# Kernel tuning notes

Measured on AMD Instinct MI355X. Metric: run time of the kernel, lower is better.

## Reference

```python
import jax, jax.numpy as jnp
import numpy as np

B, I, H = 16384, 512, 512


def setup_inputs() -> dict:
    key = jax.random.key(0)
    ks = jax.random.split(key, 10)
    inputs = jax.random.normal(ks[0], (B, I), dtype=jnp.float32)
    state = jax.random.normal(ks[1], (B, 2 * H), dtype=jnp.float32)
    # xavier_uniform for w_ih: U(-a, a), a = sqrt(6 / (fan_in + fan_out))
    a = float(np.sqrt(6.0 / (2 * H + I)))
    w_ih = jax.random.uniform(ks[2], (2 * H, I), jnp.float32, -a, a)
    b_h = jnp.zeros((H,), jnp.float32)
    pi = float(np.pi)
    d1 = jax.random.uniform(ks[3], (H,), jnp.float32, -pi, pi)
    d2 = jax.random.uniform(ks[4], (H,), jnp.float32, -pi, pi)
    d3 = jax.random.uniform(ks[5], (H,), jnp.float32, -pi, pi)
    re1 = jax.random.uniform(ks[6], (H,), jnp.float32, -1.0, 1.0)
    im1 = jax.random.uniform(ks[7], (H,), jnp.float32, -1.0, 1.0)
    re2 = jax.random.uniform(ks[8], (H,), jnp.float32, -1.0, 1.0)
    im2 = jax.random.uniform(ks[9], (H,), jnp.float32, -1.0, 1.0)
    perm = jnp.asarray(np.random.default_rng(0).permutation(H), dtype=jnp.int32)
    return {"inputs": inputs, "state": state, "w_ih": w_ih, "b_h": b_h,
            "d1": d1, "d2": d2, "d3": d3,
            "re1": re1, "im1": im1, "re2": re2, "im2": im2, "perm": perm}


def _diag_mul(w, z):
    # multiply by exp(i*w) built as complex(cos w, sin w), as in the original
    return jax.lax.complex(jnp.cos(w), jnp.sin(w)) * z


def _reflect(re, im, z):
    # z - (2/||v||^2) * (z @ conj(v)) outer v   (faithful to original matmuls)
    v = jax.lax.complex(re, im)                 # [H]
    vz = z @ jnp.conj(v)                        # [B]
    factor = 2.0 / jnp.sum(re * re + im * im)   # real scalar
    return z - factor * vz[:, None] * v[None, :]


def _modrelu(z, b):
    norm = jnp.abs(z)
    scale = jax.nn.relu(norm + b) / (norm + 1e-6)
    return z * scale


def reference(inputs, state, w_ih, b_h, d1, d2, d3, re1, im1, re2, im2, perm):
    inputs_mul = inputs @ w_ih.T                                  # [B, 2H]
    z_in = jax.lax.complex(inputs_mul[:, :H], inputs_mul[:, H:])  # [B, H] c64
    state_c = jax.lax.complex(state[:, :H], state[:, H:])
    # Unitary chain (computed in original forward, but its result `preact` is
    # never used for the returned state -- faithfully reproduced).
    s = _diag_mul(d1, state_c)
    s = jnp.fft.fft(s, axis=-1)
    s = _reflect(re1, im1, s)
    s = s[:, perm]                 # column permutation (z.T[P].T)
    s = _diag_mul(d2, s)
    s = jnp.fft.ifft(s, axis=-1)
    s = _reflect(re2, im2, s)
    s = _diag_mul(d3, s)
    preact = z_in + s              # dead in original; kept for fidelity
    new_state_c = _modrelu(z_in, b_h)
    return jnp.concatenate([jnp.real(new_state_c), jnp.imag(new_state_c)], axis=1)
```

## Files before the change

### kernel.cpp

```cpp
#include <hip/hip_runtime.h>
#include <hip/hip_bf16.h>


typedef __attribute__((ext_vector_type(8))) short bf16x8;
typedef __attribute__((ext_vector_type(4))) float f32x4;

#define BM 256
#define BK 64
#define KDIM 512
#define NDIM 1024
#define NKT (KDIM / BK)

__device__ __forceinline__ unsigned short f2bf(float f) {
    unsigned u = __builtin_bit_cast(unsigned, f);
    u += 0x7fffu + ((u >> 16) & 1u);
    return (unsigned short)(u >> 16);
}

__global__ __launch_bounds__(256) void cvt_both(
    const float* __restrict__ A, const float* __restrict__ W,
    unsigned short* __restrict__ Abf, unsigned short* __restrict__ Wbf,
    int nA4, int nTot4) {
    int i = blockIdx.x * blockDim.x + threadIdx.x;
    int stride = gridDim.x * blockDim.x;
    for (; i < nTot4; i += stride) {
        float4 v;
        if (i < nA4) v = reinterpret_cast<const float4*>(A)[i];
        else         v = reinterpret_cast<const float4*>(W)[i - nA4];
        ushort4 o;
        o.x = f2bf(v.x); o.y = f2bf(v.y); o.z = f2bf(v.z); o.w = f2bf(v.w);
        if (i < nA4) reinterpret_cast<ushort4*>(Abf)[i] = o;
        else         reinterpret_cast<ushort4*>(Wbf)[i - nA4] = o;
    }
}

__device__ __forceinline__ void gload_lds16(const void* g, void* l) {
    __builtin_amdgcn_global_load_lds(
        (const __attribute__((address_space(1))) unsigned int*)g,
        (__attribute__((address_space(3))) unsigned int*)l, 16, 0, 0);
}

__global__ __launch_bounds__(512, 2) void gemm_modrelu(
    const unsigned short* __restrict__ A,
    const unsigned short* __restrict__ W,
    const float* __restrict__ bh,
    float* __restrict__ out)
{
    __shared__ unsigned short At[2][BM * BK];
    __shared__ unsigned short Bt[2][BM * BK];

    const int tid = threadIdx.x;
    const int w   = tid >> 6;
    const int l   = tid & 63;
    const int l15 = l & 15;
    const int l4  = l >> 4;
    const int wm  = w >> 2;
    const int wn  = w & 3;

    const int bx = blockIdx.x;
    const int lg = (bx & 7) * 32 + (bx >> 3);
    const int mb = lg >> 2;
    const int cb = lg & 3;

    const int srow = l >> 3;
    const int sseg = (l & 7) ^ srow;

    const unsigned short* ga[4];
    const unsigned short* gb[4];
    int ldso[4];
#pragma unroll
    for (int is = 0; is < 4; ++is) {
        int row  = w * 32 + is * 8 + srow;
        ga[is]   = A + (size_t)(mb * BM + row) * KDIM + sseg * 8;
        int wrow = (row >> 7) * 512 + cb * 128 + (row & 127);
        gb[is]   = W + (size_t)wrow * KDIM + sseg * 8;
        ldso[is] = (w * 32 + is * 8) * BK;
    }

    f32x4 acc[8][4];
#pragma unroll
    for (int i = 0; i < 8; ++i)
#pragma unroll
        for (int j = 0; j < 4; ++j) acc[i][j] = f32x4{0.f, 0.f, 0.f, 0.f};

    auto stage = [&](int kt, int buf) {
#pragma unroll
        for (int is = 0; is < 4; ++is)
            gload_lds16(ga[is] + kt * BK, &At[buf][ldso[is]]);
#pragma unroll
        for (int is = 0; is < 4; ++is)
            gload_lds16(gb[is] + kt * BK, &Bt[buf][ldso[is]]);
    };

    stage(0, 0);
    stage(1, 1);
    asm volatile("s_waitcnt vmcnt(8)" ::: "memory");
    __builtin_amdgcn_s_barrier();

#pragma unroll
    for (int kt = 0; kt < NKT; ++kt) {
        const int buf = kt & 1;

#pragma unroll
        for (int ks = 0; ks < 2; ++ks) {
            bf16x8 af[8], bf[4];
            const int slot = (ks * 4 + l4) ^ (l15 & 7);
#pragma unroll
            for (int i = 0; i < 8; ++i) {
                int row = wm * 128 + i * 16 + l15;
                af[i] = *(const bf16x8*)(&At[buf][row * BK + slot * 8]);
            }
#pragma unroll
            for (int jn = 0; jn < 4; ++jn) {
                int row = (jn < 2) ? (wn * 32 + jn * 16 + l15)
                                   : (128 + wn * 32 + (jn - 2) * 16 + l15);
                bf[jn] = *(const bf16x8*)(&Bt[buf][row * BK + slot * 8]);
            }
            asm volatile("s_waitcnt lgkmcnt(0)" ::: "memory");
            __builtin_amdgcn_sched_barrier(0);
            __builtin_amdgcn_s_setprio(1);
#pragma unroll
            for (int i = 0; i < 8; ++i)
#pragma unroll
                for (int jn = 0; jn < 4; ++jn)
                    acc[i][jn] = __builtin_amdgcn_mfma_f32_16x16x32_bf16(
                        af[i], bf[jn], acc[i][jn], 0, 0, 0);
            __builtin_amdgcn_s_setprio(0);
        }

        __builtin_amdgcn_s_barrier();
        if (kt + 2 < NKT) stage(kt + 2, buf);
        if (kt < NKT - 1) {
            if (kt + 2 < NKT) asm volatile("s_waitcnt vmcnt(8)" ::: "memory");
            else              asm volatile("s_waitcnt vmcnt(0)" ::: "memory");
            __builtin_amdgcn_s_barrier();
        }
    }

#pragma unroll
    for (int jn = 0; jn < 2; ++jn) {
        int n = cb * 128 + wn * 32 + jn * 16 + l15;
        float b = bh[n];
#pragma unroll
        for (int i = 0; i < 8; ++i) {
#pragma unroll
            for (int j = 0; j < 4; ++j) {
                int m = mb * BM + wm * 128 + i * 16 + l4 * 4 + j;
                float re  = acc[i][jn][j];
                float imv = acc[i][jn + 2][j];
                float norm  = sqrtf(re * re + imv * imv);
                float scale = fmaxf(norm + b, 0.f) * __builtin_amdgcn_rcpf(norm + 1e-6f);
                float* po = out + (size_t)m * NDIM + n;
                __builtin_nontemporal_store(re  * scale, po);
                __builtin_nontemporal_store(imv * scale, po + 512);
            }
        }
    }
}

extern "C" void kernel_launch(void* const* d_in, const int* in_sizes, int n_in,
                              void* d_out, int out_size, void* d_ws, size_t ws_size,
                              hipStream_t stream) {
    const float* inputs = (const float*)d_in[0];
    const float* w_ih   = (const float*)d_in[2];
    const float* b_h    = (const float*)d_in[3];
    float* out = (float*)d_out;

    unsigned short* Abf = (unsigned short*)d_ws;
    unsigned short* Wbf = (unsigned short*)((char*)d_ws + (size_t)16384 * 512 * 2);

    const int nA4 = (16384 * 512) / 4;
    const int nW4 = (1024 * 512) / 4;
    cvt_both<<<2048, 256, 0, stream>>>(inputs, w_ih, Abf, Wbf, nA4, nA4 + nW4);

    gemm_modrelu<<<256, 512, 0, stream>>>(Abf, Wbf, b_h, out);
}
```

Before: 44.59 us.

## Fuse fp32-to-bf16 conversion of activations into GEMM staging through registers

Removes the separate conversion pass over the large input matrix: the GEMM now loads fp32 A tiles into registers, converts them to bf16, and writes them swizzled into LDS, while W is still preconverted. This avoids writing and rereading a bf16 copy of A in global memory. In exchange the A path loses async direct-to-LDS loads, uses more registers and VMEM waits inside the main loop, and reads twice the bytes per A tile inside the GEMM.

```diff
diff --git a/kernel.cpp b/kernel.cpp
--- a/kernel.cpp
+++ b/kernel.cpp
@@ -17,20 +17,15 @@
     return (unsigned short)(u >> 16);
 }
 
-__global__ __launch_bounds__(256) void cvt_both(
-    const float* __restrict__ A, const float* __restrict__ W,
-    unsigned short* __restrict__ Abf, unsigned short* __restrict__ Wbf,
-    int nA4, int nTot4) {
+__global__ __launch_bounds__(256) void cvt_w(const float* __restrict__ W,
+                                             unsigned short* __restrict__ Wbf, int n4) {
     int i = blockIdx.x * blockDim.x + threadIdx.x;
     int stride = gridDim.x * blockDim.x;
-    for (; i < nTot4; i += stride) {
-        float4 v;
-        if (i < nA4) v = reinterpret_cast<const float4*>(A)[i];
-        else         v = reinterpret_cast<const float4*>(W)[i - nA4];
+    for (; i < n4; i += stride) {
+        float4 v = reinterpret_cast<const float4*>(W)[i];
         ushort4 o;
         o.x = f2bf(v.x); o.y = f2bf(v.y); o.z = f2bf(v.z); o.w = f2bf(v.w);
-        if (i < nA4) reinterpret_cast<ushort4*>(Abf)[i] = o;
-        else         reinterpret_cast<ushort4*>(Wbf)[i - nA4] = o;
+        reinterpret_cast<ushort4*>(Wbf)[i] = o;
     }
 }
 
@@ -41,7 +36,7 @@
 }
 
 __global__ __launch_bounds__(512, 2) void gemm_modrelu(
-    const unsigned short* __restrict__ A,
+    const float* __restrict__ A,
     const unsigned short* __restrict__ W,
     const float* __restrict__ bh,
     float* __restrict__ out)
@@ -62,20 +57,47 @@
     const int mb = lg >> 2;
     const int cb = lg & 3;
 
+    const int arow0 = tid >> 4;
+    const int aseg  = tid & 15;
+    const int aswz  = (arow0 & 7) << 3;
+    const float4* ga[8];
+#pragma unroll
+    for (int s = 0; s < 8; ++s)
+        ga[s] = reinterpret_cast<const float4*>(
+                    A + (size_t)(mb * BM + s * 32 + arow0) * KDIM) + aseg;
+
     const int srow = l >> 3;
     const int sseg = (l & 7) ^ srow;
-
-    const unsigned short* ga[4];
     const unsigned short* gb[4];
     int ldso[4];
 #pragma unroll
     for (int is = 0; is < 4; ++is) {
         int row  = w * 32 + is * 8 + srow;
-        ga[is]   = A + (size_t)(mb * BM + row) * KDIM + sseg * 8;
         int wrow = (row >> 7) * 512 + cb * 128 + (row & 127);
         gb[is]   = W + (size_t)wrow * KDIM + sseg * 8;
         ldso[is] = (w * 32 + is * 8) * BK;
     }
+
+    float4 ra[8];
+    auto load_a = [&](int kt) {
+#pragma unroll
+        for (int s = 0; s < 8; ++s) ra[s] = ga[s][kt * (BK / 4)];
+    };
+    auto write_a = [&](int buf) {
+#pragma unroll
+        for (int s = 0; s < 8; ++s) {
+            ushort4 o;
+            o.x = f2bf(ra[s].x); o.y = f2bf(ra[s].y);
+            o.z = f2bf(ra[s].z); o.w = f2bf(ra[s].w);
+            int row = s * 32 + arow0;
+            *reinterpret_cast<ushort4*>(&At[buf][row * BK + ((aseg * 4) ^ aswz)]) = o;
+        }
+    };
+    auto stage_b = [&](int kt, int buf) {
+#pragma unroll
+        for (int is = 0; is < 4; ++is)
+            gload_lds16(gb[is] + kt * BK, &Bt[buf][ldso[is]]);
+    };
 
     f32x4 acc[8][4];
 #pragma unroll
@@ -83,38 +105,39 @@
 #pragma unroll
         for (int j = 0; j < 4; ++j) acc[i][j] = f32x4{0.f, 0.f, 0.f, 0.f};
 
-    auto stage = [&](int kt, int buf) {
-#pragma unroll
-        for (int is = 0; is < 4; ++is)
-            gload_lds16(ga[is] + kt * BK, &At[buf][ldso[is]]);
-#pragma unroll
-        for (int is = 0; is < 4; ++is)
-            gload_lds16(gb[is] + kt * BK, &Bt[buf][ldso[is]]);
-    };
-
-    stage(0, 0);
-    stage(1, 1);
-    asm volatile("s_waitcnt vmcnt(8)" ::: "memory");
+    load_a(0);
+    asm volatile("s_waitcnt vmcnt(0)" ::: "memory");
+    write_a(0);
+    stage_b(0, 0);
+    load_a(1);
+    stage_b(1, 1);
+    asm volatile("s_waitcnt vmcnt(12) lgkmcnt(0)" ::: "memory");
     __builtin_amdgcn_s_barrier();
 
 #pragma unroll
     for (int kt = 0; kt < NKT; ++kt) {
         const int buf = kt & 1;
 
+        if (kt + 1 < NKT) {
+            asm volatile("s_waitcnt vmcnt(4)" ::: "memory");
+            write_a(buf ^ 1);
+        }
+        if (kt + 2 < NKT) load_a(kt + 2);
+
 #pragma unroll
         for (int ks = 0; ks < 2; ++ks) {
             bf16x8 af[8], bf[4];
-            const int slot = (ks * 4 + l4) ^ (l15 & 7);
+            const int slot = (ks * 4 + l4);
 #pragma unroll
             for (int i = 0; i < 8; ++i) {
                 int row = wm * 128 + i * 16 + l15;
-                af[i] = *(const bf16x8*)(&At[buf][row * BK + slot * 8]);
+                af[i] = *(const bf16x8*)(&At[buf][row * BK + (slot ^ (row & 7)) * 8]);
             }
 #pragma unroll
             for (int jn = 0; jn < 4; ++jn) {
                 int row = (jn < 2) ? (wn * 32 + jn * 16 + l15)
                                    : (128 + wn * 32 + (jn - 2) * 16 + l15);
-                bf[jn] = *(const bf16x8*)(&Bt[buf][row * BK + slot * 8]);
+                bf[jn] = *(const bf16x8*)(&Bt[buf][row * BK + (slot ^ (row & 7)) * 8]);
             }
             asm volatile("s_waitcnt lgkmcnt(0)" ::: "memory");
             __builtin_amdgcn_sched_barrier(0);
@@ -128,11 +151,11 @@
             __builtin_amdgcn_s_setprio(0);
         }
 
-        __builtin_amdgcn_s_barrier();
-        if (kt + 2 < NKT) stage(kt + 2, buf);
-        if (kt < NKT - 1) {
+        if (kt + 1 < NKT) {
+            __builtin_amdgcn_s_barrier();
             if (kt + 2 < NKT) asm volatile("s_waitcnt vmcnt(8)" ::: "memory");
             else              asm volatile("s_waitcnt vmcnt(0)" ::: "memory");
+            if (kt + 2 < NKT) stage_b(kt + 2, buf);
             __builtin_amdgcn_s_barrier();
         }
     }
@@ -166,12 +189,9 @@
     const float* b_h    = (const float*)d_in[3];
     float* out = (float*)d_out;
 
-    unsigned short* Abf = (unsigned short*)d_ws;
-    unsigned short* Wbf = (unsigned short*)((char*)d_ws + (size_t)16384 * 512 * 2);
+    unsigned short* Wbf = (unsigned short*)d_ws;
 
-    const int nA4 = (16384 * 512) / 4;
-    const int nW4 = (1024 * 512) / 4;
-    cvt_both<<<2048, 256, 0, stream>>>(inputs, w_ih, Abf, Wbf, nA4, nA4 + nW4);
+    cvt_w<<<512, 256, 0, stream>>>(w_ih, Wbf, (1024 * 512) / 4);
 
-    gemm_modrelu<<<256, 512, 0, stream>>>(Abf, Wbf, b_h, out);
+    gemm_modrelu<<<256, 512, 0, stream>>>(inputs, Wbf, b_h, out);
 }
```

After: 47.55 us. 6.6% more time.

## Shrink GEMM tile to 128x128 with more blocks and stage epilogue through LDS

Applied to the files above, without the earlier changes.

Halves the M tile and the N tile per block, giving 1024 blocks of 256 threads instead of 256 blocks of 512. This is meant to fill the GPU's compute units more evenly and reduce tail imbalance. The modReLU epilogue now writes results into shared memory first, then emits coalesced 16-byte nontemporal stores instead of scattered scalar stores. The smaller tiles lower data reuse and add an extra LDS round trip and sync in the epilogue.

```diff
diff --git a/kernel.cpp b/kernel.cpp
--- a/kernel.cpp
+++ b/kernel.cpp
@@ -5,11 +5,14 @@
 typedef __attribute__((ext_vector_type(8))) short bf16x8;
 typedef __attribute__((ext_vector_type(4))) float f32x4;
 
-#define BM 256
+#define BM 128
 #define BK 64
 #define KDIM 512
 #define NDIM 1024
-#define NKT (KDIM / BK)
+#define NKT 8
+
+#define VMCNT(n) asm volatile("s_waitcnt vmcnt(" #n ")" ::: "memory")
+#define LGKM(n)  asm volatile("s_waitcnt lgkmcnt(" #n ")" ::: "memory")
 
 __device__ __forceinline__ unsigned short f2bf(float f) {
     unsigned u = __builtin_bit_cast(unsigned, f);
@@ -40,31 +43,32 @@
         (__attribute__((address_space(3))) unsigned int*)l, 16, 0, 0);
 }
 
-__global__ __launch_bounds__(512, 2) void gemm_modrelu(
+__global__ __launch_bounds__(256, 2) void gemm_modrelu(
     const unsigned short* __restrict__ A,
     const unsigned short* __restrict__ W,
     const float* __restrict__ bh,
     float* __restrict__ out)
 {
-    __shared__ unsigned short At[2][BM * BK];
-    __shared__ unsigned short Bt[2][BM * BK];
+    __shared__ __align__(16) char smem[65536];
+    unsigned short* At0 = (unsigned short*)smem;
+    unsigned short* Bt0 = (unsigned short*)(smem + 32768);
+    float* C = (float*)smem;
 
     const int tid = threadIdx.x;
     const int w   = tid >> 6;
     const int l   = tid & 63;
     const int l15 = l & 15;
     const int l4  = l >> 4;
-    const int wm  = w >> 2;
-    const int wn  = w & 3;
+    const int wm  = w >> 1;
+    const int wn  = w & 1;
 
     const int bx = blockIdx.x;
-    const int lg = (bx & 7) * 32 + (bx >> 3);
-    const int mb = lg >> 2;
-    const int cb = lg & 3;
+    const int lg = (bx & 7) * 128 + (bx >> 3);
+    const int mb = lg >> 3;
+    const int cb = lg & 7;
 
     const int srow = l >> 3;
     const int sseg = (l & 7) ^ srow;
-
     const unsigned short* ga[4];
     const unsigned short* gb[4];
     int ldso[4];
@@ -72,89 +76,107 @@
     for (int is = 0; is < 4; ++is) {
         int row  = w * 32 + is * 8 + srow;
         ga[is]   = A + (size_t)(mb * BM + row) * KDIM + sseg * 8;
-        int wrow = (row >> 7) * 512 + cb * 128 + (row & 127);
+        int wrow = (row >> 6) * 512 + cb * 64 + (row & 63);
         gb[is]   = W + (size_t)wrow * KDIM + sseg * 8;
         ldso[is] = (w * 32 + is * 8) * BK;
     }
 
-    f32x4 acc[8][4];
+    auto stage = [&](int kt, int buf) {
+        unsigned short* at = At0 + buf * (BM * BK);
+        unsigned short* bt = Bt0 + buf * (BM * BK);
 #pragma unroll
-    for (int i = 0; i < 8; ++i)
+        for (int is = 0; is < 4; ++is)
+            gload_lds16(ga[is] + kt * BK, at + ldso[is]);
+#pragma unroll
+        for (int is = 0; is < 4; ++is)
+            gload_lds16(gb[is] + kt * BK, bt + ldso[is]);
+    };
+
+    f32x4 acc[4][4];
+#pragma unroll
+    for (int i = 0; i < 4; ++i)
 #pragma unroll
         for (int j = 0; j < 4; ++j) acc[i][j] = f32x4{0.f, 0.f, 0.f, 0.f};
 
-    auto stage = [&](int kt, int buf) {
-#pragma unroll
-        for (int is = 0; is < 4; ++is)
-            gload_lds16(ga[is] + kt * BK, &At[buf][ldso[is]]);
-#pragma unroll
-        for (int is = 0; is < 4; ++is)
-            gload_lds16(gb[is] + kt * BK, &Bt[buf][ldso[is]]);
-    };
-
     stage(0, 0);
     stage(1, 1);
-    asm volatile("s_waitcnt vmcnt(8)" ::: "memory");
+    VMCNT(8);
     __builtin_amdgcn_s_barrier();
 
 #pragma unroll
     for (int kt = 0; kt < NKT; ++kt) {
         const int buf = kt & 1;
+        const unsigned short* at = At0 + buf * (BM * BK);
+        const unsigned short* bt = Bt0 + buf * (BM * BK);
 
 #pragma unroll
         for (int ks = 0; ks < 2; ++ks) {
-            bf16x8 af[8], bf[4];
-            const int slot = (ks * 4 + l4) ^ (l15 & 7);
+            bf16x8 af[4], bf[4];
 #pragma unroll
-            for (int i = 0; i < 8; ++i) {
-                int row = wm * 128 + i * 16 + l15;
-                af[i] = *(const bf16x8*)(&At[buf][row * BK + slot * 8]);
+            for (int i = 0; i < 4; ++i) {
+                int row = wm * 64 + i * 16 + l15;
+                af[i] = *(const bf16x8*)(&at[row * BK + (((ks * 4 + l4) ^ (row & 7)) * 8)]);
             }
 #pragma unroll
-            for (int jn = 0; jn < 4; ++jn) {
-                int row = (jn < 2) ? (wn * 32 + jn * 16 + l15)
-                                   : (128 + wn * 32 + (jn - 2) * 16 + l15);
-                bf[jn] = *(const bf16x8*)(&Bt[buf][row * BK + slot * 8]);
+            for (int j = 0; j < 4; ++j) {
+                int row = (j >> 1) * 64 + wn * 32 + (j & 1) * 16 + l15;
+                bf[j] = *(const bf16x8*)(&bt[row * BK + (((ks * 4 + l4) ^ (row & 7)) * 8)]);
             }
-            asm volatile("s_waitcnt lgkmcnt(0)" ::: "memory");
+            LGKM(0);
             __builtin_amdgcn_sched_barrier(0);
             __builtin_amdgcn_s_setprio(1);
 #pragma unroll
-            for (int i = 0; i < 8; ++i)
+            for (int i = 0; i < 4; ++i)
 #pragma unroll
-                for (int jn = 0; jn < 4; ++jn)
-                    acc[i][jn] = __builtin_amdgcn_mfma_f32_16x16x32_bf16(
-                        af[i], bf[jn], acc[i][jn], 0, 0, 0);
+                for (int j = 0; j < 4; ++j)
+                    acc[i][j] = __builtin_amdgcn_mfma_f32_16x16x32_bf16(
+                        af[i], bf[j], acc[i][j], 0, 0, 0);
             __builtin_amdgcn_s_setprio(0);
         }
 
-        __builtin_amdgcn_s_barrier();
-        if (kt + 2 < NKT) stage(kt + 2, buf);
-        if (kt < NKT - 1) {
-            if (kt + 2 < NKT) asm volatile("s_waitcnt vmcnt(8)" ::: "memory");
-            else              asm volatile("s_waitcnt vmcnt(0)" ::: "memory");
+        if (kt + 1 < NKT) {
+            __builtin_amdgcn_s_barrier();
+            if (kt + 2 < NKT) {
+                stage(kt + 2, buf);
+                VMCNT(8);
+            } else {
+                VMCNT(0);
+            }
             __builtin_amdgcn_s_barrier();
         }
     }
 
+    __syncthreads();
 #pragma unroll
-    for (int jn = 0; jn < 2; ++jn) {
-        int n = cb * 128 + wn * 32 + jn * 16 + l15;
-        float b = bh[n];
+    for (int j = 0; j < 2; ++j) {
+        int col = wn * 32 + j * 16 + l15;
+        float b = bh[cb * 64 + col];
 #pragma unroll
-        for (int i = 0; i < 8; ++i) {
+        for (int i = 0; i < 4; ++i) {
 #pragma unroll
-            for (int j = 0; j < 4; ++j) {
-                int m = mb * BM + wm * 128 + i * 16 + l4 * 4 + j;
-                float re  = acc[i][jn][j];
-                float imv = acc[i][jn + 2][j];
+            for (int jj = 0; jj < 4; ++jj) {
+                int rowl = wm * 64 + i * 16 + l4 * 4 + jj;
+                float re  = acc[i][j][jj];
+                float imv = acc[i][j + 2][jj];
                 float norm  = sqrtf(re * re + imv * imv);
                 float scale = fmaxf(norm + b, 0.f) * __builtin_amdgcn_rcpf(norm + 1e-6f);
-                float* po = out + (size_t)m * NDIM + n;
-                __builtin_nontemporal_store(re  * scale, po);
-                __builtin_nontemporal_store(imv * scale, po + 512);
+                C[rowl * 128 + col]      = re  * scale;
+                C[rowl * 128 + 64 + col] = imv * scale;
             }
         }
+    }
+    __syncthreads();
+
+    const int seg   = l & 31;
+    const int rhalf = l >> 5;
+#pragma unroll
+    for (int it = 0; it < 16; ++it) {
+        int rowl = w * 32 + it * 2 + rhalf;
+        f32x4 v = *reinterpret_cast<const f32x4*>(&C[rowl * 128 + seg * 4]);
+        size_t m = (size_t)(mb * BM + rowl);
+        int n = (seg < 16) ? (cb * 64 + seg * 4)
+                           : (512 + cb * 64 + (seg - 16) * 4);
+        __builtin_nontemporal_store(v, reinterpret_cast<f32x4*>(out + m * NDIM + n));
     }
 }
 
@@ -173,5 +195,5 @@
     const int nW4 = (1024 * 512) / 4;
     cvt_both<<<2048, 256, 0, stream>>>(inputs, w_ih, Abf, Wbf, nA4, nA4 + nW4);
 
-    gemm_modrelu<<<256, 512, 0, stream>>>(Abf, Wbf, b_h, out);
+    gemm_modrelu<<<1024, 256, 0, stream>>>(Abf, Wbf, b_h, out);
 }
```

After: 42.54 us. 4.6% less time.
